# Kernel optimization log

Measured on AMD Instinct MI355X. Metric: run time of the kernel, lower is better.

## Reference

```python
import jax, jax.numpy as jnp
import numpy as np

K = 3          # kernel_size
PAD = 1        # padding
HEADS = 4
C = 128
K2 = K * K


def setup_inputs() -> dict:
    key = jax.random.key(0)
    k1, k2, k3, k4 = jax.random.split(key, 4)
    B, H, W = 4, 128, 128
    x = jax.random.normal(k1, (B, H, W, C), jnp.float32)
    w_qkv = jax.random.normal(k2, (K2 * K2 * HEADS, C), jnp.float32) * 0.02
    w_v = jax.random.normal(k3, (K2, C, C), jnp.float32) * np.sqrt(2.0 / (K2 * C))
    w_proj = jax.random.normal(k4, (C, C), jnp.float32) * 0.02
    return {"x": x, "w_qkv": w_qkv, "w_v": w_v, "w_proj": w_proj}


def _csa(x, w_qkv, w_v, w_proj):
    B, H, W, Cc = x.shape
    hd = Cc // HEADS
    scale = hd ** (-0.5)
    N = H * W
    # attention map: Linear(C -> k^4*heads); pool is identity for stride=1
    att = jnp.einsum('bhwc,oc->bhwo', x, w_qkv)                      # [B,H,W,81*heads]
    att = att.reshape(B, N, HEADS, K2, K2).transpose(0, 2, 1, 3, 4)  # [B,heads,N,k2,k2]
    att = jax.nn.softmax(att * scale, axis=-1)
    # unfold x into per-location 3x3 windows (patch index p = di*K + dj)
    xp = jnp.pad(x, ((0, 0), (PAD, PAD), (PAD, PAD), (0, 0)))
    patches = jnp.stack([xp[:, di:di + H, dj:dj + W, :]
                         for di in range(K) for dj in range(K)], axis=3)  # [B,H,W,k2,C]
    v = patches.reshape(B, N, K2, Cc)
    # grouped 1x1 conv == per-window-position CxC matmul
    v = jnp.einsum('pij,bnpj->bnpi', w_v, v)                          # [B,N,k2,C]
    v = v.reshape(B, N, K2, HEADS, hd).transpose(0, 3, 1, 2, 4)       # [B,heads,N,k2,hd]
    out = jnp.einsum('bhnpq,bhnqd->bhnpd', att, v)                    # [B,heads,N,k2,hd]
    # -> [B, C, k2, H, W] with channel index = head*hd + d (matches torch fold layout)
    out = out.transpose(0, 1, 4, 3, 2).reshape(B, Cc, K2, H, W)
    # fold: scatter-add overlapping patches back to (H, W)
    acc = jnp.zeros((B, Cc, H + 2 * PAD, W + 2 * PAD), x.dtype)
    p = 0
    for di in range(K):
        for dj in range(K):
            acc = acc.at[:, :, di:di + H, dj:dj + W].add(out[:, :, p])
            p += 1
    y = acc[:, :, PAD:PAD + H, PAD:PAD + W].transpose(0, 2, 3, 1)     # [B,H,W,C]
    return jnp.einsum('bhwc,oc->bhwo', y, w_proj)


def reference(x, w_qkv, w_v, w_proj):
    return _csa(x, w_qkv, w_v, w_proj)
```

## Files before the change

### kernel.cpp

```cpp
#include <hip/hip_runtime.h>


typedef short bf16x8 __attribute__((ext_vector_type(8)));
typedef float f32x4  __attribute__((ext_vector_type(4)));
typedef float v2f    __attribute__((ext_vector_type(2)));

#define SCALE 0.17677669529663687f

__device__ __forceinline__ unsigned short f2bf(float f) {
  unsigned u = __float_as_uint(f);
  u = (u + 0x7fffu + ((u >> 16) & 1u)) >> 16;
  return (unsigned short)u;
}
__device__ __forceinline__ float bf2f(unsigned short s) {
  return __uint_as_float(((unsigned)s) << 16);
}
__device__ __forceinline__ unsigned pk2bf(float lo, float hi) {
  unsigned a = __float_as_uint(lo) + 0x8000u;
  unsigned b = __float_as_uint(hi) + 0x8000u;
  return __builtin_amdgcn_perm(b, a, 0x07060302u);
}
__device__ __forceinline__ bf16x8 ld16(const unsigned short* p) {
  union { bf16x8 v; uint4 u; } r;
  r.u = *(const uint4*)p;
  return r.v;
}

__global__ __launch_bounds__(256) void cvt_kernel(const float* __restrict__ wq,
                                                  const float* __restrict__ wv,
                                                  const float* __restrict__ wp,
                                                  unsigned short* __restrict__ wq2,
                                                  unsigned short* __restrict__ wvb2,
                                                  unsigned short* __restrict__ wpb2) {
  int i = blockIdx.x * 256 + threadIdx.x;
  if (i >= 27392) return;
  if (i < 6912) {
    int l = i & 63, rest = i >> 6;
    int kk = rest & 3, ct = rest >> 2;
    int s = ct / 3, tile = ct - s * 3;
    int row16 = l & 15, qd4 = row16 >> 2, r = row16 & 3;
    int g = s * 4 + qd4, q = tile * 4 + r;
    int k0 = kk * 32 + (l >> 4) * 8;
    unsigned short* d = wq2 + (long)i * 8;
    ushort4 o0 = make_ushort4(0, 0, 0, 0), o1 = make_ushort4(0, 0, 0, 0);
    if (q < 9) {
      int c = (g / 9) * 81 + (g % 9) * 9 + q;
      const float* sp = wq + (long)c * 128 + k0;
      float4 a = *(const float4*)sp, b = *(const float4*)(sp + 4);
      o0.x = f2bf(a.x); o0.y = f2bf(a.y); o0.z = f2bf(a.z); o0.w = f2bf(a.w);
      o1.x = f2bf(b.x); o1.y = f2bf(b.y); o1.z = f2bf(b.z); o1.w = f2bf(b.w);
    }
    *(ushort4*)d = o0;
    *(ushort4*)(d + 4) = o1;
    return;
  }
  const float* s;
  unsigned short* d;
  if (i < 25344) {
    int it = i - 6912;
    int l = it & 63, mk = it >> 6;
    int kk = mk & 3, m = (mk >> 2) & 1, qcg = mk >> 3;
    int cg = qcg & 3, q = qcg >> 2;
    int chan = cg * 32 + m * 16 + (l & 15);
    int k0 = kk * 32 + (l >> 4) * 8;
    s = wv + (long)q * 16384 + chan * 128 + k0;
    d = wvb2 + (long)it * 8;
  } else {
    int it = i - 25344;
    int l = it & 63, kk = (it >> 6) & 3, tn = it >> 8;
    int col = tn * 16 + (l & 15);
    int k0 = kk * 32 + (l >> 4) * 8;
    s = wp + (long)col * 128 + k0;
    d = wpb2 + (long)it * 8;
  }
  float4 a = *(const float4*)s, b = *(const float4*)(s + 4);
  ushort4 o0, o1;
  o0.x = f2bf(a.x); o0.y = f2bf(a.y); o0.z = f2bf(a.z); o0.w = f2bf(a.w);
  o1.x = f2bf(b.x); o1.y = f2bf(b.y); o1.z = f2bf(b.z); o1.w = f2bf(b.w);
  *(ushort4*)d = o0;
  *(ushort4*)(d + 4) = o1;
}

__global__ __launch_bounds__(512, 2) void av_kernel(const float* __restrict__ x,
                                                    const unsigned short* __restrict__ wvb2,
                                                    const unsigned short* __restrict__ wq2,
                                                    const unsigned short* __restrict__ wpb2,
                                                    float* __restrict__ out) {
  __shared__ unsigned short A[144 * 136];
  __shared__ unsigned short S[100 * 136];
  __shared__ unsigned P[18100];
  const int t = threadIdx.x;
  const int bb = blockIdx.z;
  const int r0 = blockIdx.y * 8, c0 = blockIdx.x * 8;
  const int l15 = t & 15, qd = (t >> 4) & 3, wvi = t >> 6;
  const int lane = t & 63;
  const int cg = wvi & 3, lp = wvi >> 2;
  const int n = (wvi & 3) * 16 + l15, lr = n >> 3, lc = n & 7;
  const int g = (wvi >> 2) * 4 + qd, head = g >> 1;
  const long nb = (long)bb * 16384;
  unsigned* Sdw = (unsigned*)S;
  unsigned* Adw = (unsigned*)A;

  int xbI[4];
#pragma unroll
  for (int i = 0; i < 4; i++) {
    int tile = lp * 4 + i;
    int ml = tile < 7 ? tile * 16 + l15 : 0;
    xbI[i] = (ml / 10) * 12 + (ml % 10) + 13;
  }

#pragma unroll
  for (int k = 0; k < 9; k++) {
    int i = t + k * 512;
    int row = i >> 5, seg = i & 31;
    int gr = r0 - 2 + row / 12, gc = c0 - 2 + row % 12;
    float4 v = make_float4(0.f, 0.f, 0.f, 0.f);
    if (gr >= 0 && gr < 128 && gc >= 0 && gc < 128)
      v = *(const float4*)(x + (nb + gr * 128 + gc) * 128 + seg * 4);
    *(uint2*)(Adw + row * 68 + seg * 2) = make_uint2(pk2bf(v.x, v.y), pk2bf(v.z, v.w));
  }
  __syncthreads();

#pragma unroll
  for (int k8 = 0; k8 < 8; k8++) {
    const int u = wvi * 8 + k8;
    if (u < 63) {
      const int s9 = u / 7, lt = u - s9 * 7;
      const int loc = lt * 16 + l15;
      const int l10 = loc / 10, lm = loc - l10 * 10;
      int xr = (l10 + 1) * 12 + lm + 1;
      xr = xr > 143 ? 143 : xr;
      bf16x8 bx[4];
#pragma unroll
      for (int kk = 0; kk < 4; kk++)
        bx[kk] = ld16(A + xr * 136 + kk * 32 + qd * 8);
      f32x4 ac[3];
#pragma unroll
      for (int tl = 0; tl < 3; tl++) ac[tl] = (f32x4){0.f, 0.f, 0.f, 0.f};
      const unsigned short* pq = wq2 + (size_t)s9 * 6144 + lane * 8;
#pragma unroll
      for (int tl = 0; tl < 3; tl++)
#pragma unroll
        for (int kk = 0; kk < 4; kk++) {
          bf16x8 aq = *(const bf16x8*)(pq + (tl * 4 + kk) * 512);
          ac[tl] = __builtin_amdgcn_mfma_f32_16x16x32_bf16(aq, bx[kk], ac[tl], 0, 0, 0);
        }
      const int gr = r0 - 1 + l10, gc = c0 - 1 + lm;
      float e[9], sm = 0.f;
#pragma unroll
      for (int q9 = 0; q9 < 9; q9++) {
        e[q9] = __expf(ac[q9 >> 2][q9 & 3] * SCALE);
        sm += e[q9];
      }
      float inv = (gr >= 0 && gr < 128 && gc >= 0 && gc < 128) ? 1.f / sm : 0.f;
      if (loc < 100) {
        unsigned* Pw = P + loc * 181 + (s9 * 4 + qd) * 5;
        Pw[0] = pk2bf(e[0] * inv, e[1] * inv);
        Pw[1] = pk2bf(e[2] * inv, e[3] * inv);
        Pw[2] = pk2bf(e[4] * inv, e[5] * inv);
        Pw[3] = pk2bf(e[6] * inv, e[7] * inv);
        Pw[4] = pk2bf(e[8] * inv, 0.f);
      }
    }
  }

  const unsigned short* pwv = wvb2 + cg * 4096 + lane * 8;

  v2f y2[8];
#pragma unroll
  for (int i = 0; i < 8; i++) y2[i] = (v2f){0.f, 0.f};

  bf16x8 wvf[2][4];

#define LOAD_WV(qq)                                                             \
  { _Pragma("unroll") for (int m = 0; m < 2; m++)                               \
    _Pragma("unroll") for (int kk = 0; kk < 4; kk++)                            \
      wvf[m][kk] = *(const bf16x8*)(pwv + (size_t)(qq) * 16384 +                \
                                    (m * 4 + kk) * 512); }

  LOAD_WV(0)

  for (int q = 0; q < 9; q++) {
    const int qoff = (q / 3) * 12 + (q % 3) - 13;
    __syncthreads();

#pragma unroll
    for (int i = 0; i < 4; i++) {
      const int tile = lp * 4 + i;
      if (tile < 7) {
        int xr = xbI[i] + qoff;
        xr = xr > 143 ? 143 : xr;
        bf16x8 bx[4];
#pragma unroll
        for (int kk = 0; kk < 4; kk++)
          bx[kk] = ld16(A + xr * 136 + kk * 32 + qd * 8);
        f32x4 acc[2];
#pragma unroll
        for (int m = 0; m < 2; m++) acc[m] = (f32x4){0.f, 0.f, 0.f, 0.f};
#pragma unroll
        for (int kk = 0; kk < 4; kk++)
#pragma unroll
          for (int m = 0; m < 2; m++)
            acc[m] = __builtin_amdgcn_mfma_f32_16x16x32_bf16(wvf[m][kk], bx[kk],
                                                             acc[m], 0, 0, 0);
        int loc = tile * 16 + l15;
        if (loc < 100) {
#pragma unroll
          for (int m = 0; m < 2; m++)
            *(uint2*)(Sdw + loc * 68 + cg * 16 + m * 8 + qd * 2) =
                make_uint2(pk2bf(acc[m][0], acc[m][1]),
                           pk2bf(acc[m][2], acc[m][3]));
        }
      }
    }
    __syncthreads();
    if (q < 8) { LOAD_WV(q + 1) }

    const unsigned short* Ps = (const unsigned short*)P;
    const int mlb = lr * 10 + lc + 11;
    const int hq = head * 90 + q;
#pragma unroll
    for (int p = 0; p < 9; p++) {
      const int ml = mlb + (1 - p / 3) * 10 + (1 - p % 3);
      const float a = bf2f(Ps[ml * 362 + hq + p * 10]);
      const v2f a2 = {a, a};
      const uint4* Sr = (const uint4*)(Sdw + ml * 68 + g * 8);
#pragma unroll
      for (int v4 = 0; v4 < 2; v4++) {
        const uint4 u = Sr[v4];
        v2f xv;
        const int yi = v4 * 4;
        xv.x = __uint_as_float(u.x << 16); xv.y = __uint_as_float(u.x & 0xffff0000u);
        y2[yi + 0] += a2 * xv;
        xv.x = __uint_as_float(u.y << 16); xv.y = __uint_as_float(u.y & 0xffff0000u);
        y2[yi + 1] += a2 * xv;
        xv.x = __uint_as_float(u.z << 16); xv.y = __uint_as_float(u.z & 0xffff0000u);
        y2[yi + 2] += a2 * xv;
        xv.x = __uint_as_float(u.w << 16); xv.y = __uint_as_float(u.w & 0xffff0000u);
        y2[yi + 3] += a2 * xv;
      }
    }
  }

  __syncthreads();
  unsigned short* yb = A;
  {
    uint4 pk[2];
#pragma unroll
    for (int v4 = 0; v4 < 2; v4++) {
      pk[v4].x = pk2bf(y2[v4 * 4 + 0].x, y2[v4 * 4 + 0].y);
      pk[v4].y = pk2bf(y2[v4 * 4 + 1].x, y2[v4 * 4 + 1].y);
      pk[v4].z = pk2bf(y2[v4 * 4 + 2].x, y2[v4 * 4 + 2].y);
      pk[v4].w = pk2bf(y2[v4 * 4 + 3].x, y2[v4 * 4 + 3].y);
    }
    uint4* dst = (uint4*)(Adw + n * 68 + g * 8);
    dst[0] = pk[0]; dst[1] = pk[1];
  }
  __syncthreads();
  f32x4 pacc[4] = {};
#pragma unroll
  for (int kk = 0; kk < 4; kk++) {
    bf16x8 afr = ld16(yb + ((wvi & 3) * 16 + l15) * 136 + kk * 32 + qd * 8);
#pragma unroll
    for (int tn = 0; tn < 4; tn++) {
      bf16x8 bfr = *(const bf16x8*)(wpb2 + (((wvi >> 2) * 4 + tn) * 4 + kk) * 512 +
                                    lane * 8);
      pacc[tn] = __builtin_amdgcn_mfma_f32_16x16x32_bf16(afr, bfr, pacc[tn], 0, 0, 0);
    }
  }
#pragma unroll
  for (int tn = 0; tn < 4; tn++)
#pragma unroll
    for (int r = 0; r < 4; r++) {
      int nl = (wvi & 3) * 16 + qd * 4 + r;
      int col = ((wvi >> 2) * 4 + tn) * 16 + l15;
      out[(nb + (r0 + (nl >> 3)) * 128 + (c0 + (nl & 7))) * 128 + col] = pacc[tn][r];
    }
}

extern "C" void kernel_launch(void* const* d_in, const int* in_sizes, int n_in,
                              void* d_out, int out_size, void* d_ws, size_t ws_size,
                              hipStream_t stream) {
  const float* x  = (const float*)d_in[0];
  const float* wq = (const float*)d_in[1];
  const float* wv = (const float*)d_in[2];
  const float* wp = (const float*)d_in[3];
  char* w = (char*)d_ws;
  unsigned short* wq2  = (unsigned short*)w;
  unsigned short* wvb2 = wq2 + 55296;
  unsigned short* wpb2 = wvb2 + 147456;

  cvt_kernel<<<107, 256, 0, stream>>>(wq, wv, wp, wq2, wvb2, wpb2);
  dim3 g3(16, 16, 4);
  av_kernel<<<g3, 512, 0, stream>>>(x, wvb2, wq2, wpb2, (float*)d_out);
}
```

Measured before the change: 204.5 us.

## Keep softmax probabilities in registers and stage per-q slice to shrink LDS

Replaces the full bf16 attention-probability LDS buffer with per-thread registers holding packed probabilities, writing only the slice needed for the current q into a small LDS buffer each iteration. This cuts shared memory use substantially and raises the launch-bounds occupancy hint from 2 to 4 blocks per CU, aiming to hide latency with more resident waves. In exchange it adds register pressure from the held probabilities and extra LDS stores inside the q loop, and the higher occupancy target may force spills.

```diff
diff --git a/kernel.cpp b/kernel.cpp
--- a/kernel.cpp
+++ b/kernel.cpp
@@ -81,14 +81,14 @@
   *(ushort4*)(d + 4) = o1;
 }
 
-__global__ __launch_bounds__(512, 2) void av_kernel(const float* __restrict__ x,
+__global__ __launch_bounds__(512, 4) void av_kernel(const float* __restrict__ x,
                                                     const unsigned short* __restrict__ wvb2,
                                                     const unsigned short* __restrict__ wq2,
                                                     const unsigned short* __restrict__ wpb2,
                                                     float* __restrict__ out) {
   __shared__ unsigned short A[144 * 136];
   __shared__ unsigned short S[100 * 136];
-  __shared__ unsigned P[18100];
+  __shared__ unsigned short Pq[36 * 104];
   const int t = threadIdx.x;
   const int bb = blockIdx.z;
   const int r0 = blockIdx.y * 8, c0 = blockIdx.x * 8;
@@ -121,45 +121,58 @@
   }
   __syncthreads();
 
-#pragma unroll
-  for (int k8 = 0; k8 < 8; k8++) {
-    const int u = wvi * 8 + k8;
-    if (u < 63) {
-      const int s9 = u / 7, lt = u - s9 * 7;
-      const int loc = lt * 16 + l15;
-      const int l10 = loc / 10, lm = loc - l10 * 10;
-      int xr = (l10 + 1) * 12 + lm + 1;
-      xr = xr > 143 ? 143 : xr;
-      bf16x8 bx[4];
-#pragma unroll
-      for (int kk = 0; kk < 4; kk++)
-        bx[kk] = ld16(A + xr * 136 + kk * 32 + qd * 8);
-      f32x4 ac[3];
-#pragma unroll
-      for (int tl = 0; tl < 3; tl++) ac[tl] = (f32x4){0.f, 0.f, 0.f, 0.f};
-      const unsigned short* pq = wq2 + (size_t)s9 * 6144 + lane * 8;
-#pragma unroll
-      for (int tl = 0; tl < 3; tl++)
-#pragma unroll
-        for (int kk = 0; kk < 4; kk++) {
-          bf16x8 aq = *(const bf16x8*)(pq + (tl * 4 + kk) * 512);
-          ac[tl] = __builtin_amdgcn_mfma_f32_16x16x32_bf16(aq, bx[kk], ac[tl], 0, 0, 0);
+  unsigned pr[8][4], pr8[4], pga2[4];
+  {
+    float prev_e8 = 0.f;
+    unsigned short prev_a = 0xFFFFu;
+#pragma unroll
+    for (int k8 = 0; k8 < 8; k8++) {
+      const int u = wvi * 8 + k8;
+      unsigned short a16 = 0xFFFFu;
+      float e8i = 0.f;
+      if (u < 63) {
+        const int s9 = u / 7, lt = u - s9 * 7;
+        const int loc = lt * 16 + l15;
+        const int l10 = loc / 10, lm = loc - l10 * 10;
+        int xr = (l10 + 1) * 12 + lm + 1;
+        xr = xr > 143 ? 143 : xr;
+        bf16x8 bx[4];
+#pragma unroll
+        for (int kk = 0; kk < 4; kk++)
+          bx[kk] = ld16(A + xr * 136 + kk * 32 + qd * 8);
+        f32x4 ac[3];
+#pragma unroll
+        for (int tl = 0; tl < 3; tl++) ac[tl] = (f32x4){0.f, 0.f, 0.f, 0.f};
+        const unsigned short* pq = wq2 + (size_t)s9 * 6144 + lane * 8;
+#pragma unroll
+        for (int tl = 0; tl < 3; tl++)
+#pragma unroll
+          for (int kk = 0; kk < 4; kk++) {
+            bf16x8 aq = *(const bf16x8*)(pq + (tl * 4 + kk) * 512);
+            ac[tl] = __builtin_amdgcn_mfma_f32_16x16x32_bf16(aq, bx[kk], ac[tl], 0, 0, 0);
+          }
+        const int gr = r0 - 1 + l10, gc = c0 - 1 + lm;
+        float e[9], sm = 0.f;
+#pragma unroll
+        for (int q9 = 0; q9 < 9; q9++) {
+          e[q9] = __expf(ac[q9 >> 2][q9 & 3] * SCALE);
+          sm += e[q9];
         }
-      const int gr = r0 - 1 + l10, gc = c0 - 1 + lm;
-      float e[9], sm = 0.f;
-#pragma unroll
-      for (int q9 = 0; q9 < 9; q9++) {
-        e[q9] = __expf(ac[q9 >> 2][q9 & 3] * SCALE);
-        sm += e[q9];
-      }
-      float inv = (gr >= 0 && gr < 128 && gc >= 0 && gc < 128) ? 1.f / sm : 0.f;
-      if (loc < 100) {
-        unsigned* Pw = P + loc * 181 + (s9 * 4 + qd) * 5;
-        Pw[0] = pk2bf(e[0] * inv, e[1] * inv);
-        Pw[1] = pk2bf(e[2] * inv, e[3] * inv);
-        Pw[2] = pk2bf(e[4] * inv, e[5] * inv);
-        Pw[3] = pk2bf(e[6] * inv, e[7] * inv);
-        Pw[4] = pk2bf(e[8] * inv, 0.f);
+        float inv = (gr >= 0 && gr < 128 && gc >= 0 && gc < 128) ? 1.f / sm : 0.f;
+        pr[k8][0] = pk2bf(e[0] * inv, e[1] * inv);
+        pr[k8][1] = pk2bf(e[2] * inv, e[3] * inv);
+        pr[k8][2] = pk2bf(e[4] * inv, e[5] * inv);
+        pr[k8][3] = pk2bf(e[6] * inv, e[7] * inv);
+        e8i = e[8] * inv;
+        if (loc < 100)
+          a16 = (unsigned short)((s9 * 4 + qd) * 104 + loc);
+      }
+      if (k8 & 1) {
+        pr8[k8 >> 1] = pk2bf(prev_e8, e8i);
+        pga2[k8 >> 1] = (unsigned)prev_a | ((unsigned)a16 << 16);
+      } else {
+        prev_e8 = e8i;
+        prev_a = a16;
       }
     }
   }
@@ -183,6 +196,22 @@
   for (int q = 0; q < 9; q++) {
     const int qoff = (q / 3) * 12 + (q % 3) - 13;
     __syncthreads();
+
+#pragma unroll
+    for (int k8 = 0; k8 < 8; k8++) {
+      const unsigned a16 = (pga2[k8 >> 1] >> ((k8 & 1) * 16)) & 0xFFFFu;
+      if (a16 != 0xFFFFu) {
+        unsigned short v;
+        if (q == 8) {
+          v = (unsigned short)(pr8[k8 >> 1] >> ((k8 & 1) * 16));
+        } else {
+          unsigned dw = q < 2 ? pr[k8][0]
+                      : (q < 4 ? pr[k8][1] : (q < 6 ? pr[k8][2] : pr[k8][3]));
+          v = (q & 1) ? (unsigned short)(dw >> 16) : (unsigned short)dw;
+        }
+        Pq[a16] = v;
+      }
+    }
 
 #pragma unroll
     for (int i = 0; i < 4; i++) {
@@ -216,13 +245,12 @@
     __syncthreads();
     if (q < 8) { LOAD_WV(q + 1) }
 
-    const unsigned short* Ps = (const unsigned short*)P;
     const int mlb = lr * 10 + lc + 11;
-    const int hq = head * 90 + q;
+    const int hb = head * 936;
 #pragma unroll
     for (int p = 0; p < 9; p++) {
       const int ml = mlb + (1 - p / 3) * 10 + (1 - p % 3);
-      const float a = bf2f(Ps[ml * 362 + hq + p * 10]);
+      const float a = bf2f(Pq[hb + p * 104 + ml]);
       const v2f a2 = {a, a};
       const uint4* Sr = (const uint4*)(Sdw + ml * 68 + g * 8);
 #pragma unroll
```

New measurement: 193.1 us. -5.6%, faster.
